# Kernel optimization log

Measured on AMD Instinct MI355X. Metric: run time of the kernel, lower is better.

## Reference

```python
import jax, jax.numpy as jnp
import numpy as np
from jax import lax

N_PCD, N_RGB = 5000, 15000
C_PCD, C_RGB = 32, 128
N_ANCHOR, SA_RADIUS, SA_NS = 4096, 0.1, 32
NB_RADIUS, NB_K = 0.2, 64


def _fps(xyz, npoint):
    # farthest point sampling, first index = 0 (CUDA convention)
    n = xyz.shape[0]
    def step(carry, _):
        dists, last = carry
        d = jnp.sum((xyz - xyz[last]) ** 2, axis=-1)
        dists = jnp.minimum(dists, d)
        nxt = jnp.argmax(dists).astype(jnp.int32)
        return (dists, nxt), nxt
    init = (jnp.full((n,), 1e10, xyz.dtype), jnp.int32(0))
    _, rest = lax.scan(step, init, None, length=npoint - 1)
    return jnp.concatenate([jnp.zeros((1,), jnp.int32), rest])


def _ball_query(radius, nsample, points, centers):
    # first `nsample` points within radius of each center; pad with first hit
    n = points.shape[0]
    d2 = jnp.sum((centers[:, None, :] - points[None, :, :]) ** 2, axis=-1)  # [M,N]
    key_ = jnp.where(d2 < radius * radius, jnp.arange(n, dtype=jnp.float32), float(n))
    vals, idx = lax.top_k(-key_, nsample)  # smallest in-range indices first
    valid = vals > -(float(n) - 0.5)
    return jnp.where(valid, idx, idx[:, :1])


def _detection_scores(xyz, features):
    # xyz [N,3], features [N,C]
    n = xyz.shape[0]
    nb = _ball_query(NB_RADIUS, NB_K, xyz, xyz)                       # [N,K]
    feats = jnp.concatenate([features, jnp.zeros_like(features[:1])], 0)
    nb = jnp.concatenate([nb, jnp.full((1, NB_K), n, nb.dtype)], 0)   # shadow row
    feats = feats / (jnp.max(feats) + 1e-6)
    nf = feats[nb]                                                    # [N+1,K,C]
    num = jnp.maximum(jnp.sum((nb >= 0).astype(feats.dtype), 1, keepdims=True), 1.0)
    mean = jnp.sum(nf, axis=1) / num
    local_max = jax.nn.softplus(feats - mean)
    dw_max = jnp.max(feats, axis=1, keepdims=True)
    dw_score = feats / (1e-6 + dw_max)
    return jnp.max(local_max * dw_score, axis=1)[:-1]                 # [N]


def setup_inputs() -> dict:
    key = jax.random.key(0)
    ks = jax.random.split(key, 12)
    def w(k, o, i):
        return jax.random.normal(k, (o, i), jnp.float32) * 0.05
    return {
        'pcd_xyz': jax.random.uniform(ks[0], (N_PCD, 3), jnp.float32),
        'pcd_features': jax.random.normal(ks[1], (N_PCD, C_PCD), jnp.float32),
        'rgb_xyz': jax.random.uniform(ks[2], (1, N_RGB, 3), jnp.float32),
        'rgb_features': jax.random.normal(ks[3], (1, C_RGB, N_RGB), jnp.float32),
        'sa_W1': w(ks[4], 128, 3 + C_PCD + C_RGB), 'sa_b1': jnp.zeros((128,), jnp.float32),
        'sa_W2': w(ks[5], 128, 128), 'sa_b2': jnp.zeros((128,), jnp.float32),
        'sa_W3': w(ks[6], 128, 128), 'sa_b3': jnp.zeros((128,), jnp.float32),
        'fp_W1': w(ks[7], 128, C_PCD + C_RGB + 128), 'fp_b1': jnp.zeros((128,), jnp.float32),
        'fp_W2': w(ks[8], 32, 128), 'fp_b2': jnp.zeros((32,), jnp.float32),
    }


def reference(pcd_xyz, pcd_features, rgb_xyz, rgb_features,
              sa_W1, sa_b1, sa_W2, sa_b2, sa_W3, sa_b3,
              fp_W1, fp_b1, fp_W2, fp_b2):
    rgb_xyz = rgb_xyz[0]                       # [N_rgb,3]
    rgb_feat = rgb_features[0].T               # [N_rgb,128]
    # zero-padded modality channels, then concat clouds
    pcd_exp = jnp.concatenate([pcd_features, jnp.zeros((N_PCD, C_RGB), pcd_features.dtype)], 1)
    rgb_exp = jnp.concatenate([jnp.zeros((N_RGB, C_PCD), rgb_feat.dtype), rgb_feat], 1)
    xyz = jnp.concatenate([pcd_xyz, rgb_xyz], 0)      # [N,3]
    feat = jnp.concatenate([pcd_exp, rgb_exp], 0)     # [N,160]

    # --- PointnetSAModuleVotes: FPS + ball query + shared MLP + max pool ---
    fidx = _fps(xyz, N_ANCHOR)
    new_xyz = xyz[fidx]                               # [A,3]
    nb = _ball_query(SA_RADIUS, SA_NS, xyz, new_xyz)  # [A,S]
    gxyz = (xyz[nb] - new_xyz[:, None, :]) / SA_RADIUS  # normalize_xyz
    g = jnp.concatenate([gxyz, feat[nb]], -1)          # [A,S,163]
    h = g
    for W, b in ((sa_W1, sa_b1), (sa_W2, sa_b2), (sa_W3, sa_b3)):
        h = jax.nn.relu(jnp.einsum('asc,oc->aso', h, W) + b)
    sa_feat = jnp.max(h, axis=1)                       # [A,128]

    # --- PointnetFPModule: three-NN inverse-distance interpolation + MLP ---
    d2 = jnp.sum((xyz[:, None, :] - new_xyz[None, :, :]) ** 2, -1)  # [N,A]
    negd, nn_idx = lax.top_k(-d2, 3)
    wgt = 1.0 / (-negd + 1e-8)
    wgt = wgt / jnp.sum(wgt, -1, keepdims=True)
    interp = jnp.einsum('nkc,nk->nc', sa_feat[nn_idx], wgt)         # [N,128]
    f = jnp.concatenate([interp, feat], -1)                         # [N,288]
    f = jax.nn.relu(f @ fp_W1.T + fp_b1)
    f = jax.nn.relu(f @ fp_W2.T + fp_b2)                            # [N,32]

    fp_feat = f[:N_PCD]                                             # [N_pcd,32]
    vote_scores = _detection_scores(pcd_xyz, fp_feat)               # [N_pcd]
    norm = jnp.maximum(jnp.linalg.norm(fp_feat, axis=1, keepdims=True), 1e-12)
    vote_features = fp_feat / norm
    return (pcd_xyz, vote_scores, vote_features)
```

## Files before the change

### kernel.cpp

```cpp
#include <hip/hip_runtime.h>

#define N_ALL 20000
#define NPCD  5000
#define NRGB  15000
#define CPCD  32
#define CRGB  128
#define CF    160
#define NA    4096
#define SANS  32
#define NBK   64
#define K1    163
#define K1P   168
#define HD    128
#define FPK   288
#define NSOA  20480

__global__ void prep_kernel(const float* __restrict__ pcd_xyz,
                            const float* __restrict__ pcd_feat,
                            const float* __restrict__ rgb_xyz,
                            const float* __restrict__ rgb_feat,
                            const float* __restrict__ sa_W1,
                            float* __restrict__ xyz,
                            float* __restrict__ feat,
                            float* __restrict__ W1p) {
  const int TOT = N_ALL*CF + N_ALL*3 + HD*K1P;
  for (int id = blockIdx.x*blockDim.x + threadIdx.x; id < TOT; id += gridDim.x*blockDim.x) {
    if (id < N_ALL*CF) {
      int r = id / CF, c = id - r*CF;
      float v = 0.0f;
      if (r < NPCD) { if (c < CPCD) v = pcd_feat[r*CPCD + c]; }
      else          { if (c >= CPCD) v = rgb_feat[(c - CPCD)*NRGB + (r - NPCD)]; }
      feat[id] = v;
    } else if (id < N_ALL*CF + N_ALL*3) {
      int e = id - N_ALL*CF;
      xyz[e] = (e < NPCD*3) ? pcd_xyz[e] : rgb_xyz[e - NPCD*3];
    } else {
      int e = id - (N_ALL*CF + N_ALL*3);
      int o = e / K1P, c = e - o*K1P;
      W1p[e] = (c < K1) ? sa_W1[o*K1 + c] : 0.0f;
    }
  }
}

static __device__ __forceinline__ unsigned spread4(unsigned v) {
  return (v & 1u) | ((v & 2u) << 2) | ((v & 4u) << 4) | ((v & 8u) << 6);
}
static __device__ __forceinline__ unsigned morton12(float x, float y, float z) {
  int ix = (int)(x * 16.0f); ix = ix < 0 ? 0 : (ix > 15 ? 15 : ix);
  int iy = (int)(y * 16.0f); iy = iy < 0 ? 0 : (iy > 15 ? 15 : iy);
  int iz = (int)(z * 16.0f); iz = iz < 0 ? 0 : (iz > 15 ? 15 : iz);
  return spread4((unsigned)ix) | (spread4((unsigned)iy) << 1) | (spread4((unsigned)iz) << 2);
}

__global__ void __launch_bounds__(1024) sort_kernel(const float* __restrict__ pcd_xyz,
                                                    const float* __restrict__ rgb_xyz,
                                                    float* __restrict__ xsoa,
                                                    float* __restrict__ ysoa,
                                                    float* __restrict__ zsoa,
                                                    unsigned short* __restrict__ orig16) {
  __shared__ unsigned hist[4096];
  __shared__ unsigned ssum[1024];
  const int t = threadIdx.x;
  for (int i = t; i < 4096; i += 1024) hist[i] = 0u;
  __syncthreads();
  for (int p = t; p < N_ALL; p += 1024) {
    float x, y, z;
    if (p < NPCD) { x = pcd_xyz[3*p]; y = pcd_xyz[3*p+1]; z = pcd_xyz[3*p+2]; }
    else { int q = p - NPCD; x = rgb_xyz[3*q]; y = rgb_xyz[3*q+1]; z = rgb_xyz[3*q+2]; }
    atomicAdd(&hist[morton12(x, y, z)], 1u);
  }
  __syncthreads();
  unsigned h0 = hist[4*t], h1 = hist[4*t+1], h2 = hist[4*t+2], h3 = hist[4*t+3];
  unsigned mysum = h0 + h1 + h2 + h3;
  ssum[t] = mysum;
  __syncthreads();
  for (int off = 1; off < 1024; off <<= 1) {
    unsigned add = (t >= off) ? ssum[t - off] : 0u;
    __syncthreads();
    ssum[t] += add;
    __syncthreads();
  }
  unsigned excl = ssum[t] - mysum;
  hist[4*t]   = excl;
  hist[4*t+1] = excl + h0;
  hist[4*t+2] = excl + h0 + h1;
  hist[4*t+3] = excl + h0 + h1 + h2;
  __syncthreads();
  for (int p = t; p < N_ALL; p += 1024) {
    float x, y, z;
    if (p < NPCD) { x = pcd_xyz[3*p]; y = pcd_xyz[3*p+1]; z = pcd_xyz[3*p+2]; }
    else { int q = p - NPCD; x = rgb_xyz[3*q]; y = rgb_xyz[3*q+1]; z = rgb_xyz[3*q+2]; }
    unsigned dst = atomicAdd(&hist[morton12(x, y, z)], 1u);
    xsoa[dst] = x; ysoa[dst] = y; zsoa[dst] = z; orig16[dst] = (unsigned short)p;
  }
  for (int i = N_ALL + t; i < NSOA; i += 1024) {
    xsoa[i] = 0.0f; ysoa[i] = 0.0f; zsoa[i] = 0.0f; orig16[i] = 0;
  }
}

typedef float v2f __attribute__((ext_vector_type(2)));

template <int CTRL>
static __device__ __forceinline__ float dpp_max_step(float v) {
  int b = __float_as_int(v);
  int s = __builtin_amdgcn_update_dpp(b, b, CTRL, 0xF, 0xF, false);
  return fmaxf(v, __int_as_float(s));
}

__global__ void __launch_bounds__(1024)
__attribute__((amdgpu_waves_per_eu(2, 4)))
fps_kernel(const float* __restrict__ xsoa,
           const float* __restrict__ ysoa,
           const float* __restrict__ zsoa,
           const unsigned short* __restrict__ orig16,
           const float* __restrict__ pcd_xyz,
           int* __restrict__ fidx,
           float* __restrict__ axyz) {
  #pragma clang fp contract(off)
  const int t = threadIdx.x;
  const int lane = t & 63, wv = t >> 6;
  __shared__ unsigned short lorg[NSOA];
  __shared__ float    wmax[2][16];
  __shared__ unsigned slot[2];
  for (int i = t; i < NSOA; i += 1024) lorg[i] = orig16[i];
  const int base = 20 * t;
  v2f X[10], Y[10], Z[10], D[10];
  #pragma unroll
  for (int j = 0; j < 10; j++) {
    int p = base + 2*j;
    X[j] = *(const v2f*)(xsoa + p);
    Y[j] = *(const v2f*)(ysoa + p);
    Z[j] = *(const v2f*)(zsoa + p);
    D[j].x = (p     < N_ALL) ? 1e10f : -1.0f;
    D[j].y = (p + 1 < N_ALL) ? 1e10f : -1.0f;
  }
  float blx = 1e30f, bhx = -1e30f, bly = 1e30f, bhy = -1e30f, blz = 1e30f, bhz = -1e30f;
  #pragma unroll
  for (int j = 0; j < 10; j++) {
    blx = fminf(blx, fminf(X[j].x, X[j].y)); bhx = fmaxf(bhx, fmaxf(X[j].x, X[j].y));
    bly = fminf(bly, fminf(Y[j].x, Y[j].y)); bhy = fmaxf(bhy, fmaxf(Y[j].x, Y[j].y));
    blz = fminf(blz, fminf(Z[j].x, Z[j].y)); bhz = fmaxf(bhz, fmaxf(Z[j].x, Z[j].y));
  }
  float tmaxc = (base < N_ALL) ? 1e10f : -1.0f;
  if (t == 0) { slot[0] = 0xFFFFFFFFu; slot[1] = 0xFFFFFFFFu; }
  float cx = pcd_xyz[0], cy = pcd_xyz[1], cz = pcd_xyz[2];
  if (t == 0) { fidx[0] = 0; axyz[0] = cx; axyz[1] = cy; axyz[2] = cz; }
  for (int it = 1; it < NA; ++it) {
    const int par = it & 1;
    float tdx = fmaxf(fmaxf(blx - cx, cx - bhx), 0.0f);
    float tdy = fmaxf(fmaxf(bly - cy, cy - bhy), 0.0f);
    float tdz = fmaxf(fmaxf(blz - cz, cz - bhz), 0.0f);
    float lb2 = (tdx*tdx + tdy*tdy) + tdz*tdz;
    float tmax;
    if (lb2 * 0.99f < tmaxc) {
      v2f cxv = {cx, cx}, cyv = {cy, cy}, czv = {cz, cz};
      float m[10];
      #pragma unroll
      for (int j = 0; j < 10; j++) {
        v2f dx = X[j] - cxv;
        v2f dy = Y[j] - cyv;
        v2f dz = Z[j] - czv;
        v2f d  = (dx*dx + dy*dy) + dz*dz;
        D[j].x = fminf(D[j].x, d.x);
        D[j].y = fminf(D[j].y, d.y);
        m[j] = fmaxf(D[j].x, D[j].y);
      }
      float m0 = fmaxf(m[0], m[1]), m1 = fmaxf(m[2], m[3]);
      float m2 = fmaxf(m[4], m[5]), m3 = fmaxf(m[6], m[7]);
      tmax = fmaxf(fmaxf(fmaxf(m0, m1), fmaxf(m2, m3)), fmaxf(m[8], m[9]));
      tmaxc = tmax;
    } else {
      tmax = tmaxc;
    }
    float wm = tmax;
    wm = dpp_max_step<0x111>(wm);
    wm = dpp_max_step<0x112>(wm);
    wm = dpp_max_step<0x114>(wm);
    wm = dpp_max_step<0x118>(wm);
    wm = dpp_max_step<0x142>(wm);
    wm = dpp_max_step<0x143>(wm);
    if (lane == 63) wmax[par][wv] = wm;
    __syncthreads();
    float M = wmax[par][0];
    #pragma unroll
    for (int w = 1; w < 16; w++) M = fmaxf(M, wmax[par][w]);
    if (t == 0) slot[par ^ 1] = 0xFFFFFFFFu;
    if (tmax == M) {
      unsigned bkey = 0xFFFFFFFFu;
      #pragma unroll
      for (int j = 0; j < 10; j++) {
        unsigned p0 = (unsigned)(base + 2*j);
        if (D[j].x == M) { unsigned k = ((unsigned)lorg[p0]     << 15) |  p0;      bkey = k < bkey ? k : bkey; }
        if (D[j].y == M) { unsigned k = ((unsigned)lorg[p0 + 1] << 15) | (p0 + 1); bkey = k < bkey ? k : bkey; }
      }
      atomicMin(&slot[par], bkey);
    }
    __syncthreads();
    unsigned k = slot[par];
    unsigned pos = k & 32767u;
    cx = xsoa[pos]; cy = ysoa[pos]; cz = zsoa[pos];
    if (t == 0) {
      fidx[it] = (int)(k >> 15);
      axyz[3*it] = cx; axyz[3*it+1] = cy; axyz[3*it+2] = cz;
    }
  }
}

__global__ void sa_bq_kernel(const float* __restrict__ xyz,
                             const float* __restrict__ axyz,
                             int* __restrict__ nb) {
  #pragma clang fp contract(off)
  int wv = threadIdx.x >> 6, lane = threadIdx.x & 63;
  int a = blockIdx.x*4 + wv;
  float ax = axyz[3*a], ay = axyz[3*a+1], az = axyz[3*a+2];
  int cnt = 0, my = 0;
  for (int base = 0; base < N_ALL; base += 64) {
    int p = base + lane;
    bool in = false;
    if (p < N_ALL) {
      float dx = ax - xyz[3*p], dy = ay - xyz[3*p+1], dz = az - xyz[3*p+2];
      float d2 = (dx*dx + dy*dy) + dz*dz;
      in = d2 < 0.01f;
    }
    unsigned long long mask = __ballot(in);
    while (mask && cnt < SANS) {
      int b = __builtin_ctzll(mask);
      mask &= mask - 1;
      if (cnt == lane) my = base + b;
      cnt++;
    }
    if (cnt >= SANS) break;
  }
  int f0 = __shfl(my, 0);
  if (lane < SANS) nb[a*SANS + lane] = (lane < cnt) ? my : f0;
}

__global__ void det_bq_kernel(const float* __restrict__ pxyz,
                              int* __restrict__ nb) {
  #pragma clang fp contract(off)
  int wv = threadIdx.x >> 6, lane = threadIdx.x & 63;
  int i = blockIdx.x*4 + wv;
  float ax = pxyz[3*i], ay = pxyz[3*i+1], az = pxyz[3*i+2];
  int cnt = 0, my = 0;
  for (int base = 0; base < NPCD; base += 64) {
    int p = base + lane;
    bool in = false;
    if (p < NPCD) {
      float dx = ax - pxyz[3*p], dy = ay - pxyz[3*p+1], dz = az - pxyz[3*p+2];
      float d2 = (dx*dx + dy*dy) + dz*dz;
      in = d2 < 0.04f;
    }
    unsigned long long mask = __ballot(in);
    while (mask && cnt < NBK) {
      int b = __builtin_ctzll(mask);
      mask &= mask - 1;
      if (cnt == lane) my = base + b;
      cnt++;
    }
    if (cnt >= NBK) break;
  }
  int f0 = __shfl(my, 0);
  nb[i*NBK + lane] = (lane < cnt) ? my : f0;
}

__global__ void __launch_bounds__(128) sa_mlp_kernel(const float* __restrict__ xyz,
                                                     const float* __restrict__ feat,
                                                     const float* __restrict__ axyz,
                                                     const int* __restrict__ nb,
                                                     const float* __restrict__ W1p,
                                                     const float* __restrict__ b1,
                                                     const float* __restrict__ W2,
                                                     const float* __restrict__ b2,
                                                     const float* __restrict__ W3,
                                                     const float* __restrict__ b3,
                                                     float* __restrict__ sa_feat) {
  __shared__ float g[SANS*K1P];
  __shared__ float h1[SANS*HD];
  __shared__ int nbs[SANS];
  int a = blockIdx.x, tid = threadIdx.x;
  if (tid < SANS) nbs[tid] = nb[a*SANS + tid];
  float ax = axyz[3*a], ay = axyz[3*a+1], az = axyz[3*a+2];
  __syncthreads();
  for (int e = tid; e < SANS*K1P; e += 128) {
    int s = e / K1P, c = e - s*K1P;
    float v = 0.0f;
    int p = nbs[s];
    if (c < 3) {
      float pc  = xyz[3*p + c];
      float acx = (c == 0) ? ax : ((c == 1) ? ay : az);
      v = (pc - acx) / 0.1f;
    } else if (c < K1) {
      v = feat[p*CF + (c - 3)];
    }
    g[e] = v;
  }
  __syncthreads();
  const int o = tid;
  float acc[SANS];
  #pragma unroll
  for (int s = 0; s < SANS; s++) acc[s] = b1[o];
  for (int kc = 0; kc < 21; kc++) {
    const float4* wp = (const float4*)(W1p + o*K1P + kc*8);
    float4 w0 = wp[0], w1 = wp[1];
    #pragma unroll
    for (int s = 0; s < SANS; s++) {
      const float4* gp = (const float4*)(g + s*K1P + kc*8);
      float4 g0 = gp[0], g1 = gp[1];
      acc[s] += w0.x*g0.x + w0.y*g0.y + w0.z*g0.z + w0.w*g0.w
              + w1.x*g1.x + w1.y*g1.y + w1.z*g1.z + w1.w*g1.w;
    }
  }
  #pragma unroll
  for (int s = 0; s < SANS; s++) h1[s*HD + o] = fmaxf(acc[s], 0.0f);
  __syncthreads();
  #pragma unroll
  for (int s = 0; s < SANS; s++) acc[s] = b2[o];
  for (int kc = 0; kc < 16; kc++) {
    const float4* wp = (const float4*)(W2 + o*HD + kc*8);
    float4 w0 = wp[0], w1 = wp[1];
    #pragma unroll
    for (int s = 0; s < SANS; s++) {
      const float4* gp = (const float4*)(h1 + s*HD + kc*8);
      float4 g0 = gp[0], g1 = gp[1];
      acc[s] += w0.x*g0.x + w0.y*g0.y + w0.z*g0.z + w0.w*g0.w
              + w1.x*g1.x + w1.y*g1.y + w1.z*g1.z + w1.w*g1.w;
    }
  }
  float* h2 = g;
  #pragma unroll
  for (int s = 0; s < SANS; s++) h2[s*HD + o] = fmaxf(acc[s], 0.0f);
  __syncthreads();
  #pragma unroll
  for (int s = 0; s < SANS; s++) acc[s] = b3[o];
  for (int kc = 0; kc < 16; kc++) {
    const float4* wp = (const float4*)(W3 + o*HD + kc*8);
    float4 w0 = wp[0], w1 = wp[1];
    #pragma unroll
    for (int s = 0; s < SANS; s++) {
      const float4* gp = (const float4*)(h2 + s*HD + kc*8);
      float4 g0 = gp[0], g1 = gp[1];
      acc[s] += w0.x*g0.x + w0.y*g0.y + w0.z*g0.z + w0.w*g0.w
              + w1.x*g1.x + w1.y*g1.y + w1.z*g1.z + w1.w*g1.w;
    }
  }
  float m = 0.0f;
  #pragma unroll
  for (int s = 0; s < SANS; s++) m = fmaxf(m, fmaxf(acc[s], 0.0f));
  sa_feat[a*HD + o] = m;
}

#define INSERT3(v) { if ((v) < t0){ t2=t1; t1=t0; t0=(v);} \
                     else if ((v) < t1){ t2=t1; t1=(v);} \
                     else if ((v) < t2){ t2=(v);} }

__global__ void nn_interp_kernel(const float* __restrict__ xyz,
                                 const float* __restrict__ feat,
                                 const float* __restrict__ axyz,
                                 const float* __restrict__ sa_feat,
                                 float* __restrict__ F) {
  #pragma clang fp contract(off)
  int wv = threadIdx.x >> 6, lane = threadIdx.x & 63;
  int p = blockIdx.x*4 + wv;
  float px = xyz[3*p], py = xyz[3*p+1], pz = xyz[3*p+2];
  unsigned long long t0 = ~0ull, t1 = ~0ull, t2 = ~0ull;
  for (int j = 0; j < 64; j++) {
    int a = lane + (j << 6);
    float dx = px - axyz[3*a], dy = py - axyz[3*a+1], dz = pz - axyz[3*a+2];
    float d2 = (dx*dx + dy*dy) + dz*dz;
    unsigned long long pk = ((unsigned long long)__float_as_uint(d2) << 32) | (unsigned)a;
    INSERT3(pk);
  }
  #pragma unroll
  for (int off = 1; off < 64; off <<= 1) {
    unsigned long long b0 = __shfl_xor(t0, off);
    unsigned long long b1 = __shfl_xor(t1, off);
    unsigned long long b2 = __shfl_xor(t2, off);
    INSERT3(b0); INSERT3(b1); INSERT3(b2);
  }
  float d0 = __uint_as_float((unsigned)(t0 >> 32));
  float d1 = __uint_as_float((unsigned)(t1 >> 32));
  float d2v = __uint_as_float((unsigned)(t2 >> 32));
  int a0 = (int)(t0 & 0xFFFFFFFFull), a1 = (int)(t1 & 0xFFFFFFFFull), a2 = (int)(t2 & 0xFFFFFFFFull);
  float w0 = 1.0f/(d0 + 1e-8f), w1 = 1.0f/(d1 + 1e-8f), w2 = 1.0f/(d2v + 1e-8f);
  float wsum = w0 + w1 + w2;
  w0 /= wsum; w1 /= wsum; w2 /= wsum;
  const float* s0 = sa_feat + a0*HD;
  const float* s1 = sa_feat + a1*HD;
  const float* s2 = sa_feat + a2*HD;
  float* Fr = F + p*FPK;
  Fr[lane]      = w0*s0[lane]    + w1*s1[lane]    + w2*s2[lane];
  Fr[lane + 64] = w0*s0[lane+64] + w1*s1[lane+64] + w2*s2[lane+64];
  const float* fr = feat + p*CF;
  Fr[HD + lane]      = fr[lane];
  Fr[HD + lane + 64] = fr[lane + 64];
  if (lane < 32) Fr[HD + 128 + lane] = fr[128 + lane];
}

__global__ void __launch_bounds__(128) fp1_kernel(const float* __restrict__ F,
                                                  const float* __restrict__ W,
                                                  const float* __restrict__ b,
                                                  float* __restrict__ H) {
  __shared__ float A[32*FPK];
  int base = blockIdx.x*32, tid = threadIdx.x;
  for (int e = tid; e < 32*FPK; e += 128) {
    int r = e / FPK; int gr = base + r;
    A[e] = (gr < NPCD) ? F[gr*FPK + (e - r*FPK)] : 0.0f;
  }
  __syncthreads();
  const int o = tid;
  float acc[32];
  #pragma unroll
  for (int r = 0; r < 32; r++) acc[r] = b[o];
  for (int kc = 0; kc < 36; kc++) {
    const float4* wp = (const float4*)(W + o*FPK + kc*8);
    float4 w0 = wp[0], w1 = wp[1];
    #pragma unroll
    for (int r = 0; r < 32; r++) {
      const float4* ap = (const float4*)(A + r*FPK + kc*8);
      float4 a0 = ap[0], a1 = ap[1];
      acc[r] += w0.x*a0.x + w0.y*a0.y + w0.z*a0.z + w0.w*a0.w
              + w1.x*a1.x + w1.y*a1.y + w1.z*a1.z + w1.w*a1.w;
    }
  }
  #pragma unroll
  for (int r = 0; r < 32; r++) {
    int gr = base + r;
    if (gr < NPCD) H[gr*HD + o] = fmaxf(acc[r], 0.0f);
  }
}

__global__ void __launch_bounds__(256) fp2_kernel(const float* __restrict__ Hin,
                                                  const float* __restrict__ W,
                                                  const float* __restrict__ b,
                                                  float* __restrict__ fpf,
                                                  unsigned* __restrict__ gmax) {
  if (blockIdx.x == 0 && threadIdx.x == 0) *gmax = 0u;
  __shared__ float A[32*HD];
  int base = blockIdx.x*32, tid = threadIdx.x;
  for (int e = tid; e < 32*HD; e += 256) {
    int r = e >> 7; int gr = base + r;
    A[e] = (gr < NPCD) ? Hin[gr*HD + (e & 127)] : 0.0f;
  }
  __syncthreads();
  int o = tid & 31, rg = tid >> 5;
  float acc[4];
  #pragma unroll
  for (int j = 0; j < 4; j++) acc[j] = b[o];
  for (int kc = 0; kc < 16; kc++) {
    const float4* wp = (const float4*)(W + o*HD + kc*8);
    float4 w0 = wp[0], w1 = wp[1];
    #pragma unroll
    for (int j = 0; j < 4; j++) {
      int r = rg + (j << 3);
      const float4* ap = (const float4*)(A + r*HD + kc*8);
      float4 a0 = ap[0], a1 = ap[1];
      acc[j] += w0.x*a0.x + w0.y*a0.y + w0.z*a0.z + w0.w*a0.w
              + w1.x*a1.x + w1.y*a1.y + w1.z*a1.z + w1.w*a1.w;
    }
  }
  #pragma unroll
  for (int j = 0; j < 4; j++) {
    int gr = base + rg + (j << 3);
    if (gr < NPCD) fpf[gr*CPCD + o] = fmaxf(acc[j], 0.0f);
  }
}

__global__ void gmax_kernel(const float* __restrict__ fpf, unsigned* __restrict__ gmax) {
  int id = blockIdx.x*256 + threadIdx.x;
  float m = (id < NPCD*CPCD) ? fpf[id] : 0.0f;
  #pragma unroll
  for (int off = 1; off < 64; off <<= 1) m = fmaxf(m, __shfl_xor(m, off));
  if ((threadIdx.x & 63) == 0) atomicMax(gmax, __float_as_uint(m));
}

__global__ void det_score_kernel(const float* __restrict__ fpf,
                                 const int* __restrict__ nbd,
                                 const unsigned* __restrict__ gmax,
                                 float* __restrict__ outs) {
  int wv = threadIdx.x >> 6, lane = threadIdx.x & 63;
  int i = blockIdx.x*4 + wv;
  float g = __uint_as_float(*gmax);
  float scale = 1.0f / (g + 1e-6f);
  int c = lane & 31, h = lane >> 5;
  float sum = 0.0f;
  const int* nbr = nbd + i*NBK + h*32;
  for (int k = 0; k < 32; k++) {
    int idx = nbr[k];
    sum += fpf[idx*CPCD + c];
  }
  sum += __shfl_xor(sum, 32);
  float mean = (sum * scale) * 0.015625f;
  float fi = fpf[i*CPCD + c] * scale;
  float x = fi - mean;
  float lm = fmaxf(x, 0.0f) + log1pf(expf(-fabsf(x)));
  float dm = fi;
  #pragma unroll
  for (int off = 1; off < 64; off <<= 1) dm = fmaxf(dm, __shfl_xor(dm, off));
  float dw = fi / (1e-6f + dm);
  float pr = lm * dw;
  #pragma unroll
  for (int off = 1; off < 64; off <<= 1) pr = fmaxf(pr, __shfl_xor(pr, off));
  if (lane == 0) outs[i] = pr;
}

__global__ void vote_out_kernel(const float* __restrict__ pcd_xyz,
                                const float* __restrict__ fpf,
                                float* __restrict__ dout) {
  int id = blockIdx.x*256 + threadIdx.x;
  if (id < NPCD*3) dout[id] = pcd_xyz[id];
  int r = id - NPCD*3;
  if (r >= 0 && r < NPCD) {
    float ss = 0.0f;
    const float* fr = fpf + r*CPCD;
    #pragma unroll
    for (int cc = 0; cc < CPCD; cc++) ss += fr[cc]*fr[cc];
    float nrm = fmaxf(sqrtf(ss), 1e-12f);
    float* vf = dout + NPCD*3 + NPCD + r*CPCD;
    #pragma unroll
    for (int cc = 0; cc < CPCD; cc++) vf[cc] = fr[cc] / nrm;
  }
}

extern "C" void kernel_launch(void* const* d_in, const int* in_sizes, int n_in,
                              void* d_out, int out_size, void* d_ws, size_t ws_size,
                              hipStream_t stream) {
  const float* pcd_xyz      = (const float*)d_in[0];
  const float* pcd_features = (const float*)d_in[1];
  const float* rgb_xyz      = (const float*)d_in[2];
  const float* rgb_features = (const float*)d_in[3];
  const float* sa_W1 = (const float*)d_in[4];
  const float* sa_b1 = (const float*)d_in[5];
  const float* sa_W2 = (const float*)d_in[6];
  const float* sa_b2 = (const float*)d_in[7];
  const float* sa_W3 = (const float*)d_in[8];
  const float* sa_b3 = (const float*)d_in[9];
  const float* fp_W1 = (const float*)d_in[10];
  const float* fp_b1 = (const float*)d_in[11];
  const float* fp_W2 = (const float*)d_in[12];
  const float* fp_b2 = (const float*)d_in[13];
  float* out = (float*)d_out;

  float* xyz  = (float*)d_ws;
  float* feat = xyz  + 60000;
  float* W1p  = feat + 3200000;
  float* axyz = W1p  + 21504;
  float* saf  = axyz + 12288;
  float* F    = saf  + 524288;
  float* Hb   = F    + 1440000;
  float* fpf  = Hb   + 640000;
  int*   fidx = (int*)(fpf + 160000);
  int*   nbsa = fidx + 4096;
  int*   nbdet= nbsa + 131072;
  unsigned* gmaxp = (unsigned*)(nbdet + 320000);
  float* xsoa = (float*)(gmaxp + 1);
  float* ysoa = xsoa + NSOA;
  float* zsoa = ysoa + NSOA;
  unsigned short* orig16 = (unsigned short*)(zsoa + NSOA);

  prep_kernel<<<2048, 256, 0, stream>>>(pcd_xyz, pcd_features, rgb_xyz, rgb_features,
                                        sa_W1, xyz, feat, W1p);
  sort_kernel<<<1, 1024, 0, stream>>>(pcd_xyz, rgb_xyz, xsoa, ysoa, zsoa, orig16);
  fps_kernel<<<1, 1024, 0, stream>>>(xsoa, ysoa, zsoa, orig16, pcd_xyz, fidx, axyz);
  sa_bq_kernel<<<1024, 256, 0, stream>>>(xyz, axyz, nbsa);
  sa_mlp_kernel<<<4096, 128, 0, stream>>>(xyz, feat, axyz, nbsa, W1p, sa_b1,
                                          sa_W2, sa_b2, sa_W3, sa_b3, saf);
  nn_interp_kernel<<<1250, 256, 0, stream>>>(xyz, feat, axyz, saf, F);
  fp1_kernel<<<157, 128, 0, stream>>>(F, fp_W1, fp_b1, Hb);
  fp2_kernel<<<157, 256, 0, stream>>>(Hb, fp_W2, fp_b2, fpf, gmaxp);
  det_bq_kernel<<<1250, 256, 0, stream>>>(pcd_xyz, nbdet);
  gmax_kernel<<<625, 256, 0, stream>>>(fpf, gmaxp);
  det_score_kernel<<<1250, 256, 0, stream>>>(fpf, nbdet, gmaxp, out + NPCD*3);
  vote_out_kernel<<<79, 256, 0, stream>>>(pcd_xyz, fpf, out);
}
```

Baseline: 6.464 ms.

## Replace two-barrier FPS argmax with single-barrier packed 64-bit atomicMin

The FPS loop used two block barriers per iteration: one for a wave-max exchange through shared memory, then another after a shared atomicMin of index keys. It now packs the inverted distance bits and the precomputed index key into one 64-bit value, reduces it within each wave using DPP min passes, and issues a single 64-bit shared atomicMin per wave into a 4-slot ring. That leaves one barrier per iteration. Per-point keys are precomputed into registers rather than read from a shared orig array, which costs more registers and adds a second DPP reduction and a 64-bit atomic per iteration.

```diff
diff --git a/kernel.cpp b/kernel.cpp
--- a/kernel.cpp
+++ b/kernel.cpp
@@ -101,10 +101,10 @@
 typedef float v2f __attribute__((ext_vector_type(2)));
 
 template <int CTRL>
-static __device__ __forceinline__ float dpp_max_step(float v) {
-  int b = __float_as_int(v);
-  int s = __builtin_amdgcn_update_dpp(b, b, CTRL, 0xF, 0xF, false);
-  return fmaxf(v, __int_as_float(s));
+static __device__ __forceinline__ unsigned dpp_min_u32(unsigned v) {
+  int s = __builtin_amdgcn_update_dpp((int)v, (int)v, CTRL, 0xF, 0xF, false);
+  unsigned u = (unsigned)s;
+  return v < u ? v : u;
 }
 
 __global__ void __launch_bounds__(1024)
@@ -118,13 +118,12 @@
            float* __restrict__ axyz) {
   #pragma clang fp contract(off)
   const int t = threadIdx.x;
-  const int lane = t & 63, wv = t >> 6;
-  __shared__ unsigned short lorg[NSOA];
-  __shared__ float    wmax[2][16];
-  __shared__ unsigned slot[2];
-  for (int i = t; i < NSOA; i += 1024) lorg[i] = orig16[i];
+  const int lane = t & 63;
+  __shared__ unsigned long long ls[4];
+  if (t < 4) ls[t] = ~0ull;
   const int base = 20 * t;
   v2f X[10], Y[10], Z[10], D[10];
+  unsigned idk[20];
   #pragma unroll
   for (int j = 0; j < 10; j++) {
     int p = base + 2*j;
@@ -133,6 +132,8 @@
     Z[j] = *(const v2f*)(zsoa + p);
     D[j].x = (p     < N_ALL) ? 1e10f : -1.0f;
     D[j].y = (p + 1 < N_ALL) ? 1e10f : -1.0f;
+    idk[2*j]   = ((unsigned)orig16[p]     << 15) | (unsigned)p;
+    idk[2*j+1] = ((unsigned)orig16[p + 1] << 15) | (unsigned)(p + 1);
   }
   float blx = 1e30f, bhx = -1e30f, bly = 1e30f, bhy = -1e30f, blz = 1e30f, bhz = -1e30f;
   #pragma unroll
@@ -142,16 +143,16 @@
     blz = fminf(blz, fminf(Z[j].x, Z[j].y)); bhz = fmaxf(bhz, fmaxf(Z[j].x, Z[j].y));
   }
   float tmaxc = (base < N_ALL) ? 1e10f : -1.0f;
-  if (t == 0) { slot[0] = 0xFFFFFFFFu; slot[1] = 0xFFFFFFFFu; }
+  unsigned invd = 0xFFFFFFFFu, k32 = 0xFFFFFFFFu;
   float cx = pcd_xyz[0], cy = pcd_xyz[1], cz = pcd_xyz[2];
   if (t == 0) { fidx[0] = 0; axyz[0] = cx; axyz[1] = cy; axyz[2] = cz; }
+  __syncthreads();
   for (int it = 1; it < NA; ++it) {
-    const int par = it & 1;
+    const int s = it & 3;
     float tdx = fmaxf(fmaxf(blx - cx, cx - bhx), 0.0f);
     float tdy = fmaxf(fmaxf(bly - cy, cy - bhy), 0.0f);
     float tdz = fmaxf(fmaxf(blz - cz, cz - bhz), 0.0f);
     float lb2 = (tdx*tdx + tdy*tdy) + tdz*tdz;
-    float tmax;
     if (lb2 * 0.99f < tmaxc) {
       v2f cxv = {cx, cx}, cyv = {cy, cy}, czv = {cz, cz};
       float m[10];
@@ -167,40 +168,43 @@
       }
       float m0 = fmaxf(m[0], m[1]), m1 = fmaxf(m[2], m[3]);
       float m2 = fmaxf(m[4], m[5]), m3 = fmaxf(m[6], m[7]);
-      tmax = fmaxf(fmaxf(fmaxf(m0, m1), fmaxf(m2, m3)), fmaxf(m[8], m[9]));
+      float tmax = fmaxf(fmaxf(fmaxf(m0, m1), fmaxf(m2, m3)), fmaxf(m[8], m[9]));
       tmaxc = tmax;
-    } else {
-      tmax = tmaxc;
-    }
-    float wm = tmax;
-    wm = dpp_max_step<0x111>(wm);
-    wm = dpp_max_step<0x112>(wm);
-    wm = dpp_max_step<0x114>(wm);
-    wm = dpp_max_step<0x118>(wm);
-    wm = dpp_max_step<0x142>(wm);
-    wm = dpp_max_step<0x143>(wm);
-    if (lane == 63) wmax[par][wv] = wm;
-    __syncthreads();
-    float M = wmax[par][0];
-    #pragma unroll
-    for (int w = 1; w < 16; w++) M = fmaxf(M, wmax[par][w]);
-    if (t == 0) slot[par ^ 1] = 0xFFFFFFFFu;
-    if (tmax == M) {
-      unsigned bkey = 0xFFFFFFFFu;
+      invd = ~__float_as_uint(tmax);
+      unsigned kk = 0xFFFFFFFFu;
       #pragma unroll
       for (int j = 0; j < 10; j++) {
-        unsigned p0 = (unsigned)(base + 2*j);
-        if (D[j].x == M) { unsigned k = ((unsigned)lorg[p0]     << 15) |  p0;      bkey = k < bkey ? k : bkey; }
-        if (D[j].y == M) { unsigned k = ((unsigned)lorg[p0 + 1] << 15) | (p0 + 1); bkey = k < bkey ? k : bkey; }
+        unsigned c0 = (D[j].x == tmax) ? idk[2*j]     : 0xFFFFFFFFu;
+        unsigned c1 = (D[j].y == tmax) ? idk[2*j + 1] : 0xFFFFFFFFu;
+        unsigned cm = c0 < c1 ? c0 : c1;
+        kk = kk < cm ? kk : cm;
       }
-      atomicMin(&slot[par], bkey);
-    }
+      k32 = kk;
+    }
+    unsigned wi = invd;
+    wi = dpp_min_u32<0x111>(wi);
+    wi = dpp_min_u32<0x112>(wi);
+    wi = dpp_min_u32<0x114>(wi);
+    wi = dpp_min_u32<0x118>(wi);
+    wi = dpp_min_u32<0x142>(wi);
+    wi = dpp_min_u32<0x143>(wi);
+    unsigned wmin = (unsigned)__builtin_amdgcn_readlane((int)wi, 63);
+    unsigned sel = (invd == wmin) ? k32 : 0xFFFFFFFFu;
+    sel = dpp_min_u32<0x111>(sel);
+    sel = dpp_min_u32<0x112>(sel);
+    sel = dpp_min_u32<0x114>(sel);
+    sel = dpp_min_u32<0x118>(sel);
+    sel = dpp_min_u32<0x142>(sel);
+    sel = dpp_min_u32<0x143>(sel);
+    if (lane == 63)
+      atomicMin(&ls[s], ((unsigned long long)wmin << 32) | (unsigned long long)sel);
+    if (t == 0) ls[(it + 2) & 3] = ~0ull;
     __syncthreads();
-    unsigned k = slot[par];
-    unsigned pos = k & 32767u;
+    unsigned lo = (unsigned)ls[s];
+    unsigned pos = lo & 32767u;
     cx = xsoa[pos]; cy = ysoa[pos]; cz = zsoa[pos];
     if (t == 0) {
-      fidx[it] = (int)(k >> 15);
+      fidx[it] = (int)(lo >> 15);
       axyz[3*it] = cx; axyz[3*it+1] = cy; axyz[3*it+2] = cz;
     }
   }
```

Result: faster. 5.425 ms (-16.1%).
